# Kernel optimization log

Measured on AMD Instinct MI355X. Metric: run time of the kernel, lower is better.

## Reference

```python
import jax, jax.numpy as jnp
import numpy as np

B, H, W, C = 2, 256, 256, 256
P0, P1 = 8, 8
R0, R1 = H // P0, W // P1            # 32, 32 -> 1024 global tokens
NH = 8
DH = C // NH
MID = 4 * C                          # mlp_ratio = 4
HD = C * P0 * P1                     # high_dim = 16384
EPS = 1e-5


def _rel_index(Wh, Ww):
    # standard Swin-style relative position index, shape (Wh*Ww, Wh*Ww)
    coords = np.stack(np.meshgrid(np.arange(Wh), np.arange(Ww), indexing='ij'))
    coords = coords.reshape(2, -1)
    rel = coords[:, :, None] - coords[:, None, :]          # 2, N, N
    rel = rel.transpose(1, 2, 0).astype(np.int64)
    rel[:, :, 0] += Wh - 1
    rel[:, :, 1] += Ww - 1
    rel[:, :, 0] *= 2 * Ww - 1
    return rel.sum(-1)

_RPI = _rel_index(R0, R1)            # global branch: window_size = patch_res


def _ln(x, g, b):
    m = jnp.mean(x, axis=-1, keepdims=True)
    v = jnp.mean((x - m) ** 2, axis=-1, keepdims=True)
    return (x - m) * jax.lax.rsqrt(v + EPS) * g + b


def setup_inputs() -> dict:
    key = jax.random.key(0)
    ks = jax.random.split(key, 12)
    s = 0.02
    n_rel = (2 * R0 - 1) * (2 * R1 - 1)
    return {
        'x': jax.random.normal(ks[0], (B, H, W, C), jnp.float32),
        'ln1_g': jnp.ones((C,), jnp.float32), 'ln1_b': jnp.zeros((C,), jnp.float32),
        'ln2_g': jnp.ones((C,), jnp.float32), 'ln2_b': jnp.zeros((C,), jnp.float32),
        'rpe_table': jax.random.normal(ks[1], (n_rel, NH), jnp.float32) * s,
        'w_down': jax.random.normal(ks[2], (C, HD), jnp.float32) * s,
        'b_down': jnp.zeros((C,), jnp.float32),
        'w_up': jax.random.normal(ks[3], (HD, C), jnp.float32) * s,
        'b_up': jnp.zeros((HD,), jnp.float32),
        'w_qkv': jax.random.normal(ks[4], (3 * C, C), jnp.float32) * s,
        'b_qkv': jnp.zeros((3 * C,), jnp.float32),
        'w_proj': jax.random.normal(ks[5], (C, C), jnp.float32) * s,
        'b_proj': jnp.zeros((C,), jnp.float32),
        'w_fc1': jax.random.normal(ks[6], (MID, C), jnp.float32) * s,
        'b_fc1': jnp.zeros((MID,), jnp.float32),
        'w_fc2': jax.random.normal(ks[7], (C, MID), jnp.float32) * s,
        'b_fc2': jnp.zeros((C,), jnp.float32),
    }


def _block(x, ln1_g, ln1_b, ln2_g, ln2_b, rpe_table, w_down, b_down, w_up, b_up,
           w_qkv, b_qkv, w_proj, b_proj, w_fc1, b_fc1, w_fc2, b_fc2):
    shortcut = x
    y = _ln(x, ln1_g, ln1_b)
    # unfold + rearrange 'B (C P0 P1) (R0 R1) -> B (R0 R1) (P0 P1 C)'
    y = y.reshape(B, R0, P0, R1, P1, C).transpose(0, 1, 3, 2, 4, 5)
    y = y.reshape(B, R0 * R1, HD)                       # (B, L, high_dim)
    y = y @ w_down.T + b_down                           # (B, L, C)
    # relative position bias (NH, L, L)
    rpe = rpe_table[_RPI].transpose(2, 0, 1)
    # windowed multi-head self-attention
    L = R0 * R1
    qkv = (y @ w_qkv.T + b_qkv).reshape(B, L, 3, NH, DH).transpose(2, 0, 3, 1, 4)
    q, k, v = qkv[0], qkv[1], qkv[2]                    # (B, NH, L, DH)
    scale = DH ** -0.5
    attn = jnp.einsum('bhnd,bhmd->bhnm', q, k) * scale + rpe
    attn = jax.nn.softmax(attn, axis=-1)
    o = jnp.einsum('bhnm,bhmd->bhnd', attn, v)
    o = o.transpose(0, 2, 1, 3).reshape(B, L, C)
    o = o @ w_proj.T + b_proj
    y = o @ w_up.T + b_up                               # (B, L, high_dim)
    # fold back: (B, R0, R1, P0, P1, C) -> (B, H, W, C)
    y = y.reshape(B, R0, R1, P0, P1, C).transpose(0, 1, 3, 2, 4, 5).reshape(B, H, W, C)
    x = shortcut + y
    h = _ln(x, ln2_g, ln2_b)
    h = jax.nn.gelu(h @ w_fc1.T + b_fc1, approximate=False) @ w_fc2.T + b_fc2
    return x + h


def reference(x, ln1_g, ln1_b, ln2_g, ln2_b, rpe_table, w_down, b_down, w_up, b_up,
              w_qkv, b_qkv, w_proj, b_proj, w_fc1, b_fc1, w_fc2, b_fc2):
    return _block(x, ln1_g, ln1_b, ln2_g, ln2_b, rpe_table, w_down, b_down, w_up,
                  b_up, w_qkv, b_qkv, w_proj, b_proj, w_fc1, b_fc1, w_fc2, b_fc2)
```

## Files before the change

kernel.cpp:

```cpp
#include <hip/hip_runtime.h>

typedef __attribute__((ext_vector_type(8))) __bf16 bf16x8;
typedef __attribute__((ext_vector_type(4))) float f32x4;

#define MFMA16(a, b, c) __builtin_amdgcn_mfma_f32_16x16x32_bf16((a), (b), (c), 0, 0, 0)

#define ASYNC16(g, l) __builtin_amdgcn_global_load_lds( \
    (const __attribute__((address_space(1))) unsigned int*)(g), \
    (__attribute__((address_space(3))) unsigned int*)(l), 16, 0, 0)

__device__ __forceinline__ unsigned short f2bf(float f) {
    return __builtin_bit_cast(unsigned short, (__bf16)f);
}

__device__ __forceinline__ float wave_sum(float v) {
#pragma unroll
    for (int off = 32; off; off >>= 1) v += __shfl_xor(v, off, 64);
    return v;
}

__device__ __forceinline__ float gelu_fast(float v) {
    float z = v * fmaf(v * v, 0.0713548162f, 1.5957691216f);
    float e = __expf(-z);
    return v * __builtin_amdgcn_rcpf(1.f + e);
}

__global__ __launch_bounds__(256) void k_pre(const float* __restrict__ wdown, const float* __restrict__ wup,
                                             const float* __restrict__ wqkv, const float* __restrict__ wproj,
                                             const float* __restrict__ wfc1, const float* __restrict__ wfc2,
                                             unsigned short* __restrict__ dwdown, unsigned short* __restrict__ dwup,
                                             unsigned short* __restrict__ dwqkv, unsigned short* __restrict__ dwproj,
                                             unsigned short* __restrict__ dwfc1, unsigned short* __restrict__ dwfc2,
                                             const float* __restrict__ x, const float* __restrict__ g,
                                             const float* __restrict__ b, unsigned short* __restrict__ xln) {
    int bid = blockIdx.x;
    if (bid < 8960) {
        int i = (bid * 256 + threadIdx.x) * 4;
        const float* s; unsigned short* d; int off;
        if (i < 4194304)      { s = wdown; d = dwdown; off = i; }
        else if (i < 8388608) { s = wup;   d = dwup;   off = i - 4194304; }
        else if (i < 8585216) { s = wqkv;  d = dwqkv;  off = i - 8388608; }
        else if (i < 8650752) { s = wproj; d = dwproj; off = i - 8585216; }
        else if (i < 8912896) { s = wfc1;  d = dwfc1;  off = i - 8650752; }
        else                  { s = wfc2;  d = dwfc2;  off = i - 8912896; }
        float4 v = *reinterpret_cast<const float4*>(s + off);
        ushort4 o;
        o.x = f2bf(v.x); o.y = f2bf(v.y); o.z = f2bf(v.z); o.w = f2bf(v.w);
        *reinterpret_cast<ushort4*>(d + off) = o;
    } else {
        int wave = threadIdx.x >> 6, lane = threadIdx.x & 63;
        long long pix = (long long)(bid - 8960) * 4 + wave;
        const float* row = x + pix * 256;
        float4 v = *reinterpret_cast<const float4*>(row + lane * 4);
        float s = v.x + v.y + v.z + v.w;
        float s2 = v.x * v.x + v.y * v.y + v.z * v.z + v.w * v.w;
        s = wave_sum(s); s2 = wave_sum(s2);
        float mean = s * (1.f / 256.f);
        float rstd = rsqrtf(s2 * (1.f / 256.f) - mean * mean + 1e-5f);
        float4 gg = *reinterpret_cast<const float4*>(g + lane * 4);
        float4 bb = *reinterpret_cast<const float4*>(b + lane * 4);
        ushort4 ov;
        ov.x = f2bf((v.x - mean) * rstd * gg.x + bb.x);
        ov.y = f2bf((v.y - mean) * rstd * gg.y + bb.y);
        ov.z = f2bf((v.z - mean) * rstd * gg.z + bb.z);
        ov.w = f2bf((v.w - mean) * rstd * gg.w + bb.w);
        *reinterpret_cast<ushort4*>(xln + pix * 256 + lane * 4) = ov;
    }
}

__global__ __launch_bounds__(256, 2) void k_gemm_down2(const unsigned short* __restrict__ xln,
                                                       const unsigned short* __restrict__ wd,
                                                       float* __restrict__ part) {
    __shared__ alignas(16) unsigned short As[128 * 64];
    __shared__ alignas(16) unsigned short Bs[128 * 64];
    int wave = threadIdx.x >> 6, lane = threadIdx.x & 63, quad = lane >> 4, l16 = lane & 15;
    int mt = blockIdx.x * 128, nt = blockIdx.y * 128, k0 = blockIdx.z * 1024;
    int wm = wave & 1, wn = wave >> 1;
    int srow = wave * 32 + (lane >> 3);
    int schunk = lane & 7;
    f32x4 acc[4][4] = {};
    for (int s = 0; s < 16; s++) {
        int kg = k0 + s * 64;
        int p0 = kg >> 11, p1 = (kg >> 8) & 7, cbase = kg & 255;
#pragma unroll
        for (int i = 0; i < 4; i++) {
            int row = srow + i * 8;
            int m = mt + row;
            int bb = m >> 10, r0 = (m >> 5) & 31, r1 = m & 31;
            int c = cbase + ((schunk ^ (row & 7)) << 3);
            const unsigned short* g = xln +
                ((((long long)(bb * 256 + r0 * 8 + p0)) * 256 + (r1 * 8 + p1)) << 8) + c;
            ASYNC16(g, &As[(wave * 32 + i * 8) * 64]);
        }
#pragma unroll
        for (int i = 0; i < 4; i++) {
            int row = srow + i * 8;
            int n = nt + row;
            const unsigned short* g = wd + (long long)n * 16384 + kg + ((schunk ^ (row & 7)) << 3);
            ASYNC16(g, &Bs[(wave * 32 + i * 8) * 64]);
        }
        __syncthreads();
#pragma unroll
        for (int sub = 0; sub < 2; sub++) {
            int c = sub * 4 + quad;
            bf16x8 af[4], bfr[4];
#pragma unroll
            for (int mi = 0; mi < 4; mi++) {
                int row = wm * 64 + mi * 16 + l16;
                af[mi] = *reinterpret_cast<const bf16x8*>(&As[row * 64 + ((c ^ (row & 7)) << 3)]);
            }
#pragma unroll
            for (int ni = 0; ni < 4; ni++) {
                int row = wn * 64 + ni * 16 + l16;
                bfr[ni] = *reinterpret_cast<const bf16x8*>(&Bs[row * 64 + ((c ^ (row & 7)) << 3)]);
            }
#pragma unroll
            for (int mi = 0; mi < 4; mi++)
#pragma unroll
                for (int ni = 0; ni < 4; ni++)
                    acc[mi][ni] = MFMA16(af[mi], bfr[ni], acc[mi][ni]);
        }
        __syncthreads();
    }
    float* pb = part + (long long)blockIdx.z * 524288;
#pragma unroll
    for (int mi = 0; mi < 4; mi++)
#pragma unroll
        for (int ni = 0; ni < 4; ni++) {
            int n = nt + wn * 64 + ni * 16 + l16;
#pragma unroll
            for (int r = 0; r < 4; r++) {
                int m = mt + wm * 64 + mi * 16 + quad * 4 + r;
                pb[(long long)m * 256 + n] = acc[mi][ni][r];
            }
        }
}

__global__ __launch_bounds__(256) void k_red(const float* __restrict__ part,
                                             const float* __restrict__ bd,
                                             unsigned short* __restrict__ y) {
    int i = (blockIdx.x * 256 + threadIdx.x) * 4;
    float4 s = {0.f, 0.f, 0.f, 0.f};
#pragma unroll
    for (int p = 0; p < 16; p++) {
        float4 v = *reinterpret_cast<const float4*>(part + (long long)p * 524288 + i);
        s.x += v.x; s.y += v.y; s.z += v.z; s.w += v.w;
    }
    int n = i & 255;
    float4 bb = *reinterpret_cast<const float4*>(bd + n);
    ushort4 o;
    o.x = f2bf(s.x + bb.x); o.y = f2bf(s.y + bb.y);
    o.z = f2bf(s.z + bb.z); o.w = f2bf(s.w + bb.w);
    *reinterpret_cast<ushort4*>(y + i) = o;
}

__global__ __launch_bounds__(256) void k_gemm_qkv(const unsigned short* __restrict__ yd,
                                                  const unsigned short* __restrict__ wq,
                                                  const float* __restrict__ bq,
                                                  unsigned short* __restrict__ q,
                                                  unsigned short* __restrict__ k,
                                                  unsigned short* __restrict__ vT) {
    int wave = threadIdx.x >> 6, lane = threadIdx.x & 63, quad = lane >> 4, l16 = lane & 15;
    int m0 = blockIdx.x * 64 + wave * 16;
    int n0 = blockIdx.y * 64;
    const unsigned short* arow = yd + (long long)(m0 + l16) * 256;
    f32x4 acc[4] = {};
    for (int kb = 0; kb < 256; kb += 32) {
        bf16x8 a = *reinterpret_cast<const bf16x8*>(arow + kb + quad * 8);
#pragma unroll
        for (int ni = 0; ni < 4; ni++) {
            bf16x8 bv = *reinterpret_cast<const bf16x8*>(wq + (long long)(n0 + ni * 16 + l16) * 256 + kb + quad * 8);
            acc[ni] = MFMA16(a, bv, acc[ni]);
        }
    }
#pragma unroll
    for (int ni = 0; ni < 4; ni++) {
        int n = n0 + ni * 16 + l16;
        float bias = bq[n];
        int t = n >> 8, h = (n >> 5) & 7, d = n & 31;
#pragma unroll
        for (int r = 0; r < 4; r++) {
            int m = m0 + quad * 4 + r;
            int bh = ((m >> 10) << 3) | h;
            int l = m & 1023;
            unsigned short val = f2bf(acc[ni][r] + bias);
            if (t == 0)      q[((long long)bh * 1024 + l) * 32 + d] = val;
            else if (t == 1) k[((long long)bh * 1024 + l) * 32 + d] = val;
            else             vT[((long long)bh * 32 + d) * 1024 + l] = val;
        }
    }
}

__global__ __launch_bounds__(256) void k_attn(const unsigned short* __restrict__ q,
                                              const unsigned short* __restrict__ k,
                                              const unsigned short* __restrict__ vT,
                                              const float* __restrict__ rpe,
                                              unsigned short* __restrict__ o) {
    __shared__ alignas(16) char Pl[4][16 * 128];
    int wave = threadIdx.x >> 6, lane = threadIdx.x & 63, quad = lane >> 4, l16 = lane & 15;
    int bh = blockIdx.y, h = bh & 7;
    int m0 = blockIdx.x * 64 + wave * 16;
    const unsigned short* qb = q + (long long)bh * 32768;
    const unsigned short* kb = k + (long long)bh * 32768;
    const unsigned short* vb = vT + (long long)bh * 32768;
    char* pl = Pl[wave];
    const float scale = 0.17677669529663687f;
    int qi = m0 + l16;
    int qi0 = qi >> 5, qi1 = qi & 31;
    bf16x8 bq = *reinterpret_cast<const bf16x8*>(qb + qi * 32 + quad * 8);
    f32x4 o0 = {0.f, 0.f, 0.f, 0.f}, o1 = {0.f, 0.f, 0.f, 0.f};
    float m_run = -3.0e38f, l_run = 0.f;
    int swz = (l16 & 7) << 4;
    for (int t = 0; t < 16; t++) {
        f32x4 st[4];
        __builtin_amdgcn_s_setprio(1);
#pragma unroll
        for (int ni = 0; ni < 4; ni++) {
            bf16x8 ak = *reinterpret_cast<const bf16x8*>(kb + (t * 64 + ni * 16 + l16) * 32 + quad * 8);
            f32x4 z = {0.f, 0.f, 0.f, 0.f};
            st[ni] = MFMA16(ak, bq, z);
        }
        __builtin_amdgcn_s_setprio(0);
        float vals[16];
        float tmax = -3.0e38f;
#pragma unroll
        for (int ni = 0; ni < 4; ni++)
#pragma unroll
            for (int r = 0; r < 4; r++) {
                int kj = t * 64 + ni * 16 + quad * 4 + r;
                int kj0 = kj >> 5, kj1 = kj & 31;
                int idx = (qi0 - kj0 + 31) * 63 + (qi1 - kj1 + 31);
                float sv = st[ni][r] * scale + rpe[idx * 8 + h];
                vals[ni * 4 + r] = sv;
                tmax = fmaxf(tmax, sv);
            }
        tmax = fmaxf(tmax, __shfl_xor(tmax, 16, 64));
        tmax = fmaxf(tmax, __shfl_xor(tmax, 32, 64));
        float m_new = fmaxf(m_run, tmax);
        float fac = __expf(m_run - m_new);
        float tsum = 0.f;
#pragma unroll
        for (int ni = 0; ni < 4; ni++) {
            ushort4 w4;
            float p0v = __expf(vals[ni * 4 + 0] - m_new);
            float p1v = __expf(vals[ni * 4 + 1] - m_new);
            float p2v = __expf(vals[ni * 4 + 2] - m_new);
            float p3v = __expf(vals[ni * 4 + 3] - m_new);
            tsum += p0v + p1v + p2v + p3v;
            w4.x = f2bf(p0v); w4.y = f2bf(p1v); w4.z = f2bf(p2v); w4.w = f2bf(p3v);
            *reinterpret_cast<ushort4*>(pl + l16 * 128 + ((ni * 32 + quad * 8) ^ swz)) = w4;
        }
        tsum += __shfl_xor(tsum, 16, 64);
        tsum += __shfl_xor(tsum, 32, 64);
        l_run = l_run * fac + tsum;
        m_run = m_new;
#pragma unroll
        for (int r = 0; r < 4; r++) { o0[r] *= fac; o1[r] *= fac; }
#pragma unroll
        for (int kk = 0; kk < 2; kk++) {
            bf16x8 pb = *reinterpret_cast<const bf16x8*>(pl + l16 * 128 + ((kk * 64 + quad * 16) ^ swz));
            bf16x8 av0 = *reinterpret_cast<const bf16x8*>(vb + (long long)(l16) * 1024 + t * 64 + kk * 32 + quad * 8);
            bf16x8 av1 = *reinterpret_cast<const bf16x8*>(vb + (long long)(16 + l16) * 1024 + t * 64 + kk * 32 + quad * 8);
            __builtin_amdgcn_s_setprio(1);
            o0 = MFMA16(av0, pb, o0);
            o1 = MFMA16(av1, pb, o1);
            __builtin_amdgcn_s_setprio(0);
        }
    }
    float inv = 1.f / l_run;
    int b_ = bh >> 3;
    long long base = ((long long)(b_ * 1024 + qi)) * 256 + h * 32;
    ushort4 w0, w1;
    w0.x = f2bf(o0[0] * inv); w0.y = f2bf(o0[1] * inv);
    w0.z = f2bf(o0[2] * inv); w0.w = f2bf(o0[3] * inv);
    w1.x = f2bf(o1[0] * inv); w1.y = f2bf(o1[1] * inv);
    w1.z = f2bf(o1[2] * inv); w1.w = f2bf(o1[3] * inv);
    *reinterpret_cast<ushort4*>(o + base + quad * 4) = w0;
    *reinterpret_cast<ushort4*>(o + base + 16 + quad * 4) = w1;
}

__global__ __launch_bounds__(256) void k_gemm_proj(const unsigned short* __restrict__ a_,
                                                   const unsigned short* __restrict__ w,
                                                   const float* __restrict__ bias,
                                                   unsigned short* __restrict__ y) {
    int wave = threadIdx.x >> 6, lane = threadIdx.x & 63, quad = lane >> 4, l16 = lane & 15;
    int m0 = blockIdx.x * 64 + wave * 16;
    int n0 = blockIdx.y * 64;
    const unsigned short* arow = a_ + (long long)(m0 + l16) * 256;
    f32x4 acc[4] = {};
    for (int kb = 0; kb < 256; kb += 32) {
        bf16x8 a = *reinterpret_cast<const bf16x8*>(arow + kb + quad * 8);
#pragma unroll
        for (int ni = 0; ni < 4; ni++) {
            bf16x8 bv = *reinterpret_cast<const bf16x8*>(w + (long long)(n0 + ni * 16 + l16) * 256 + kb + quad * 8);
            acc[ni] = MFMA16(a, bv, acc[ni]);
        }
    }
#pragma unroll
    for (int ni = 0; ni < 4; ni++) {
        int n = n0 + ni * 16 + l16;
        float bv = bias[n];
#pragma unroll
        for (int r = 0; r < 4; r++)
            y[(long long)(m0 + quad * 4 + r) * 256 + n] = f2bf(acc[ni][r] + bv);
    }
}

__global__ __launch_bounds__(256) void k_up_fold(const unsigned short* __restrict__ a_,
                                                 const unsigned short* __restrict__ w,
                                                 const float* __restrict__ bup,
                                                 const float* __restrict__ x,
                                                 float* __restrict__ out) {
    __shared__ alignas(16) unsigned short Bs[128 * 256];
    int wave = threadIdx.x >> 6, lane = threadIdx.x & 63, quad = lane >> 4, l16 = lane & 15;
    int n0 = blockIdx.x * 128;
    int mbase = blockIdx.y * 512;
#pragma unroll
    for (int i = 0; i < 16; i++) {
        int R = i * 8 + wave * 2;
        int r = R + (lane >> 5);
        int cg = (lane & 31) ^ (r & 7);
        const unsigned short* g = w + (long long)(n0 + r) * 256 + cg * 8;
        ASYNC16(g, &Bs[R * 256]);
    }
    __syncthreads();
    float bias8[8];
#pragma unroll
    for (int ni = 0; ni < 8; ni++) bias8[ni] = bup[n0 + ni * 16 + l16];
    for (int s = 0; s < 8; s++) {
        int mr = mbase + s * 64 + wave * 16;
        const unsigned short* arow = a_ + (long long)(mr + l16) * 256;
        f32x4 acc[8] = {};
#pragma unroll
        for (int kb = 0; kb < 8; kb++) {
            bf16x8 a = *reinterpret_cast<const bf16x8*>(arow + kb * 32 + quad * 8);
#pragma unroll
            for (int ni = 0; ni < 8; ni++) {
                int nr = ni * 16 + l16;
                bf16x8 bv = *reinterpret_cast<const bf16x8*>(
                    &Bs[nr * 256 + (((kb * 4 + quad) ^ (nr & 7)) << 3)]);
                acc[ni] = MFMA16(a, bv, acc[ni]);
            }
        }
#pragma unroll
        for (int ni = 0; ni < 8; ni++) {
            int n = n0 + ni * 16 + l16;
            int p0 = n >> 11, p1 = (n >> 8) & 7, c = n & 255;
#pragma unroll
            for (int r = 0; r < 4; r++) {
                int m = mr + quad * 4 + r;
                int bb = m >> 10, r0 = (m >> 5) & 31, r1 = m & 31;
                long long addr = ((long long)bb << 24) + (long long)(r0 * 8 + p0) * 65536 + (r1 * 8 + p1) * 256 + c;
                out[addr] = x[addr] + acc[ni][r] + bias8[ni];
            }
        }
    }
}

#define LP 264
__global__ __launch_bounds__(512, 4) void k_mlp(float* __restrict__ xio,
                                                const float* __restrict__ g2,
                                                const float* __restrict__ b2,
                                                const unsigned short* __restrict__ w1,
                                                const float* __restrict__ bfc1,
                                                const unsigned short* __restrict__ w2,
                                                const float* __restrict__ bfc2) {
    __shared__ unsigned short Aln[64 * LP];
    __shared__ unsigned short Hc[64 * LP];
    int wave = threadIdx.x >> 6, lane = threadIdx.x & 63, quad = lane >> 4, l16 = lane & 15;
    long long m0 = (long long)blockIdx.x * 64;
    float4 gg = *reinterpret_cast<const float4*>(g2 + lane * 4);
    float4 bb = *reinterpret_cast<const float4*>(b2 + lane * 4);
#pragma unroll
    for (int i = 0; i < 8; i++) {
        int p = wave * 8 + i;
        float4 v = *reinterpret_cast<const float4*>(xio + (m0 + p) * 256 + lane * 4);
        float s = v.x + v.y + v.z + v.w;
        float s2 = v.x * v.x + v.y * v.y + v.z * v.z + v.w * v.w;
        s = wave_sum(s); s2 = wave_sum(s2);
        float mean = s * (1.f / 256.f);
        float rstd = rsqrtf(s2 * (1.f / 256.f) - mean * mean + 1e-5f);
        ushort4 o;
        o.x = f2bf((v.x - mean) * rstd * gg.x + bb.x);
        o.y = f2bf((v.y - mean) * rstd * gg.y + bb.y);
        o.z = f2bf((v.z - mean) * rstd * gg.z + bb.z);
        o.w = f2bf((v.w - mean) * rstd * gg.w + bb.w);
        *reinterpret_cast<ushort4*>(&Aln[p * LP + lane * 4]) = o;
    }
    __syncthreads();
    f32x4 acc2[4][2] = {};
    for (int ch = 0; ch < 4; ch++) {
        f32x4 acc1[4][2] = {};
#pragma unroll
        for (int kb = 0; kb < 256; kb += 32) {
            bf16x8 af[4];
#pragma unroll
            for (int mi = 0; mi < 4; mi++)
                af[mi] = *reinterpret_cast<const bf16x8*>(&Aln[(mi * 16 + l16) * LP + kb + quad * 8]);
#pragma unroll
            for (int ni = 0; ni < 2; ni++) {
                bf16x8 bv = *reinterpret_cast<const bf16x8*>(w1 + (long long)(ch * 256 + wave * 32 + ni * 16 + l16) * 256 + kb + quad * 8);
                __builtin_amdgcn_s_setprio(1);
#pragma unroll
                for (int mi = 0; mi < 4; mi++)
                    acc1[mi][ni] = MFMA16(af[mi], bv, acc1[mi][ni]);
                __builtin_amdgcn_s_setprio(0);
            }
        }
#pragma unroll
        for (int ni = 0; ni < 2; ni++) {
            int n = ch * 256 + wave * 32 + ni * 16 + l16;
            float bias = bfc1[n];
            int col = wave * 32 + ni * 16 + l16;
#pragma unroll
            for (int mi = 0; mi < 4; mi++) {
#pragma unroll
                for (int r = 0; r < 4; r++) {
                    float vv = acc1[mi][ni][r] + bias;
                    Hc[(mi * 16 + quad * 4 + r) * LP + col] = f2bf(gelu_fast(vv));
                }
            }
        }
        __syncthreads();
#pragma unroll
        for (int kb = 0; kb < 256; kb += 32) {
            bf16x8 af[4];
#pragma unroll
            for (int mi = 0; mi < 4; mi++)
                af[mi] = *reinterpret_cast<const bf16x8*>(&Hc[(mi * 16 + l16) * LP + kb + quad * 8]);
#pragma unroll
            for (int ni = 0; ni < 2; ni++) {
                bf16x8 bv = *reinterpret_cast<const bf16x8*>(w2 + (long long)(wave * 32 + ni * 16 + l16) * 1024 + ch * 256 + kb + quad * 8);
                __builtin_amdgcn_s_setprio(1);
#pragma unroll
                for (int mi = 0; mi < 4; mi++)
                    acc2[mi][ni] = MFMA16(af[mi], bv, acc2[mi][ni]);
                __builtin_amdgcn_s_setprio(0);
            }
        }
        __syncthreads();
    }
#pragma unroll
    for (int ni = 0; ni < 2; ni++) {
        int n = wave * 32 + ni * 16 + l16;
        float bias = bfc2[n];
#pragma unroll
        for (int mi = 0; mi < 4; mi++) {
#pragma unroll
            for (int r = 0; r < 4; r++) {
                long long row = m0 + mi * 16 + quad * 4 + r;
                float xv = xio[row * 256 + n];
                xio[row * 256 + n] = xv + acc2[mi][ni][r] + bias;
            }
        }
    }
}

extern "C" void kernel_launch(void* const* d_in, const int* in_sizes, int n_in,
                              void* d_out, int out_size, void* d_ws, size_t ws_size,
                              hipStream_t stream) {
    const float* x      = (const float*)d_in[0];
    const float* ln1_g  = (const float*)d_in[1];
    const float* ln1_b  = (const float*)d_in[2];
    const float* ln2_g  = (const float*)d_in[3];
    const float* ln2_b  = (const float*)d_in[4];
    const float* rpe    = (const float*)d_in[5];
    const float* w_down = (const float*)d_in[6];
    const float* b_down = (const float*)d_in[7];
    const float* w_up   = (const float*)d_in[8];
    const float* b_up   = (const float*)d_in[9];
    const float* w_qkv  = (const float*)d_in[10];
    const float* b_qkv  = (const float*)d_in[11];
    const float* w_proj = (const float*)d_in[12];
    const float* b_proj = (const float*)d_in[13];
    const float* w_fc1  = (const float*)d_in[14];
    const float* b_fc1  = (const float*)d_in[15];
    const float* w_fc2  = (const float*)d_in[16];
    const float* b_fc2  = (const float*)d_in[17];
    float* out = (float*)d_out;

    char* wp = (char*)d_ws;
    auto alloc = [&](size_t bytes) { void* p = (void*)wp; wp += (bytes + 255) & ~(size_t)255; return p; };
    unsigned short* wdown_bf = (unsigned short*)alloc(4194304 * 2);
    unsigned short* wup_bf   = (unsigned short*)alloc(4194304 * 2);
    unsigned short* wqkv_bf  = (unsigned short*)alloc(196608 * 2);
    unsigned short* wproj_bf = (unsigned short*)alloc(65536 * 2);
    unsigned short* wfc1_bf  = (unsigned short*)alloc(262144 * 2);
    unsigned short* wfc2_bf  = (unsigned short*)alloc(262144 * 2);
    unsigned short* ydown    = (unsigned short*)alloc(524288 * 2);
    unsigned short* qb       = (unsigned short*)alloc(524288 * 2);
    unsigned short* kb       = (unsigned short*)alloc(524288 * 2);
    unsigned short* vT       = (unsigned short*)alloc(524288 * 2);
    unsigned short* obf      = (unsigned short*)alloc(524288 * 2);
    unsigned short* oproj    = (unsigned short*)alloc(524288 * 2);

    unsigned short* xln = (unsigned short*)d_out;
    float* part         = (float*)((char*)d_out + 100663296);

    k_pre<<<41728, 256, 0, stream>>>(w_down, w_up, w_qkv, w_proj, w_fc1, w_fc2,
                                     wdown_bf, wup_bf, wqkv_bf, wproj_bf, wfc1_bf, wfc2_bf,
                                     x, ln1_g, ln1_b, xln);
    k_gemm_down2<<<dim3(16, 2, 16), 256, 0, stream>>>(xln, wdown_bf, part);
    k_red<<<512, 256, 0, stream>>>(part, b_down, ydown);
    k_gemm_qkv<<<dim3(32, 12), 256, 0, stream>>>(ydown, wqkv_bf, b_qkv, qb, kb, vT);
    k_attn<<<dim3(16, 16), 256, 0, stream>>>(qb, kb, vT, rpe, obf);
    k_gemm_proj<<<dim3(32, 4), 256, 0, stream>>>(obf, wproj_bf, b_proj, oproj);
    k_up_fold<<<dim3(128, 4), 256, 0, stream>>>(oproj, wup_bf, b_up, x, out);
    k_mlp<<<2048, 512, 0, stream>>>(out, ln2_g, ln2_b, wfc1_bf, b_fc1, wfc2_bf, b_fc2);
}
```

Baseline: 504.9 us.

## Software-pipeline MLP fc1/fc2 chunks with double-buffered hidden tile

Restructures the fused MLP kernel to process the hidden dimension in 8 chunks of 128 instead of 4 of 256. The hidden tile is double-buffered, so fc1+GELU for the next chunk is interleaved with fc2 MMAs on the current chunk, and only one barrier per chunk is needed instead of two. This is meant to overlap the two GEMM phases and cut synchronization stalls. In exchange it adds loop overhead and more MFMA instructions per iteration, which raises register pressure, and it removes the setprio hints.

After: 494.0 us, median of 2. -2.2%, faster.

```diff
diff --git a/kernel.cpp b/kernel.cpp
--- a/kernel.cpp
+++ b/kernel.cpp
@@ -358,6 +358,7 @@
 }
 
 #define LP 264
+#define LH 136
 __global__ __launch_bounds__(512, 4) void k_mlp(float* __restrict__ xio,
                                                 const float* __restrict__ g2,
                                                 const float* __restrict__ b2,
@@ -366,7 +367,7 @@
                                                 const unsigned short* __restrict__ w2,
                                                 const float* __restrict__ bfc2) {
     __shared__ unsigned short Aln[64 * LP];
-    __shared__ unsigned short Hc[64 * LP];
+    __shared__ unsigned short Hc[2][64 * LH];
     int wave = threadIdx.x >> 6, lane = threadIdx.x & 63, quad = lane >> 4, l16 = lane & 15;
     long long m0 = (long long)blockIdx.x * 64;
     float4 gg = *reinterpret_cast<const float4*>(g2 + lane * 4);
@@ -388,57 +389,68 @@
         *reinterpret_cast<ushort4*>(&Aln[p * LP + lane * 4]) = o;
     }
     __syncthreads();
+    int col = wave * 16 + l16;
+    {
+        f32x4 acc1[4] = {};
+        const unsigned short* w1c = w1 + (long long)(wave * 16 + l16) * 256;
+#pragma unroll
+        for (int kb = 0; kb < 256; kb += 32) {
+            bf16x8 bv = *reinterpret_cast<const bf16x8*>(w1c + kb + quad * 8);
+#pragma unroll
+            for (int mi = 0; mi < 4; mi++) {
+                bf16x8 aa = *reinterpret_cast<const bf16x8*>(&Aln[(mi * 16 + l16) * LP + kb + quad * 8]);
+                acc1[mi] = MFMA16(aa, bv, acc1[mi]);
+            }
+        }
+        float bias = bfc1[wave * 16 + l16];
+#pragma unroll
+        for (int mi = 0; mi < 4; mi++)
+#pragma unroll
+            for (int r = 0; r < 4; r++)
+                Hc[0][(mi * 16 + quad * 4 + r) * LH + col] = f2bf(gelu_fast(acc1[mi][r] + bias));
+    }
     f32x4 acc2[4][2] = {};
-    for (int ch = 0; ch < 4; ch++) {
-        f32x4 acc1[4][2] = {};
-#pragma unroll
-        for (int kb = 0; kb < 256; kb += 32) {
-            bf16x8 af[4];
+    for (int ch = 0; ch < 8; ch++) {
+        __syncthreads();
+        int cur = ch & 1;
+        const unsigned short* w2c = w2 + (long long)(wave * 32) * 1024 + ch * 128;
+        const unsigned short* w1n = w1 + (long long)(((ch + 1) & 7) * 128 + wave * 16 + l16) * 256;
+        bool do1 = (ch < 7);
+        f32x4 nacc1[4] = {};
+#pragma unroll
+        for (int s = 0; s < 4; s++) {
+            bf16x8 ah[4];
 #pragma unroll
             for (int mi = 0; mi < 4; mi++)
-                af[mi] = *reinterpret_cast<const bf16x8*>(&Aln[(mi * 16 + l16) * LP + kb + quad * 8]);
+                ah[mi] = *reinterpret_cast<const bf16x8*>(&Hc[cur][(mi * 16 + l16) * LH + s * 32 + quad * 8]);
 #pragma unroll
             for (int ni = 0; ni < 2; ni++) {
-                bf16x8 bv = *reinterpret_cast<const bf16x8*>(w1 + (long long)(ch * 256 + wave * 32 + ni * 16 + l16) * 256 + kb + quad * 8);
-                __builtin_amdgcn_s_setprio(1);
+                bf16x8 bv = *reinterpret_cast<const bf16x8*>(w2c + (long long)(ni * 16 + l16) * 1024 + s * 32 + quad * 8);
 #pragma unroll
                 for (int mi = 0; mi < 4; mi++)
-                    acc1[mi][ni] = MFMA16(af[mi], bv, acc1[mi][ni]);
-                __builtin_amdgcn_s_setprio(0);
-            }
-        }
-#pragma unroll
-        for (int ni = 0; ni < 2; ni++) {
-            int n = ch * 256 + wave * 32 + ni * 16 + l16;
-            float bias = bfc1[n];
-            int col = wave * 32 + ni * 16 + l16;
-#pragma unroll
-            for (int mi = 0; mi < 4; mi++) {
-#pragma unroll
-                for (int r = 0; r < 4; r++) {
-                    float vv = acc1[mi][ni][r] + bias;
-                    Hc[(mi * 16 + quad * 4 + r) * LP + col] = f2bf(gelu_fast(vv));
+                    acc2[mi][ni] = MFMA16(ah[mi], bv, acc2[mi][ni]);
+            }
+            if (do1) {
+#pragma unroll
+                for (int t = 0; t < 2; t++) {
+                    int kb = (s * 2 + t) * 32;
+                    bf16x8 bv = *reinterpret_cast<const bf16x8*>(w1n + kb + quad * 8);
+#pragma unroll
+                    for (int mi = 0; mi < 4; mi++) {
+                        bf16x8 aa = *reinterpret_cast<const bf16x8*>(&Aln[(mi * 16 + l16) * LP + kb + quad * 8]);
+                        nacc1[mi] = MFMA16(aa, bv, nacc1[mi]);
+                    }
                 }
             }
         }
-        __syncthreads();
-#pragma unroll
-        for (int kb = 0; kb < 256; kb += 32) {
-            bf16x8 af[4];
+        if (do1) {
+            float bias = bfc1[(ch + 1) * 128 + wave * 16 + l16];
 #pragma unroll
             for (int mi = 0; mi < 4; mi++)
-                af[mi] = *reinterpret_cast<const bf16x8*>(&Hc[(mi * 16 + l16) * LP + kb + quad * 8]);
-#pragma unroll
-            for (int ni = 0; ni < 2; ni++) {
-                bf16x8 bv = *reinterpret_cast<const bf16x8*>(w2 + (long long)(wave * 32 + ni * 16 + l16) * 1024 + ch * 256 + kb + quad * 8);
-                __builtin_amdgcn_s_setprio(1);
-#pragma unroll
-                for (int mi = 0; mi < 4; mi++)
-                    acc2[mi][ni] = MFMA16(af[mi], bv, acc2[mi][ni]);
-                __builtin_amdgcn_s_setprio(0);
-            }
-        }
-        __syncthreads();
+#pragma unroll
+                for (int r = 0; r < 4; r++)
+                    Hc[cur ^ 1][(mi * 16 + quad * 4 + r) * LH + col] = f2bf(gelu_fast(nacc1[mi][r] + bias));
+        }
     }
 #pragma unroll
     for (int ni = 0; ni < 2; ni++) {
```
